# Performance work log

Hardware: AMD Instinct MI355X
Metric: run time of the kernel (lower is better)

Reference implementation:

```python
import jax, jax.numpy as jnp
import numpy as np

M, K, N, GROUP = 32, 8192, 28672, 128


def setup_inputs() -> dict:
    key = jax.random.key(0)
    k1, k2, k3, k4 = jax.random.split(key, 4)
    x = jax.random.normal(k1, (M, K), dtype=jnp.float16)
    # int32 words, each packing 8 consecutive int4 values along K
    qweight = jax.random.randint(k2, (K // 8, N), 0, 2147483647, dtype=jnp.int32)
    scales = (jax.random.uniform(k3, (K // GROUP, N), dtype=jnp.float32) * 0.01 + 0.001).astype(jnp.float16)
    bias = (jax.random.normal(k4, (N,), dtype=jnp.float32) * 0.02).astype(jnp.float16)
    return {"x": x, "qweight": qweight, "scales": scales, "bias": bias}


def reference(x, qweight, scales, bias):
    # Unpack 8 int4 nibbles per int32 word along K: (K//8, N) -> (K, N)
    K8, n = qweight.shape
    shifts = (jnp.arange(8, dtype=jnp.int32) * 4)[None, :, None]
    wq = ((qweight[:, None, :] >> shifts) & 15).reshape(K8 * 8, n)  # [K, N] in [0,15]
    # Dequant: zero-point fixed at 8 (pack() asserts zeros==8), per-group scales
    w = wq.astype(jnp.float16) - jnp.float16(8.0)
    g, gs = scales.shape[0], (K8 * 8) // scales.shape[0]
    w = (w.reshape(g, gs, n) * scales[:, None, :]).reshape(K8 * 8, n)  # [K, N] fp16
    return jnp.dot(x, w) + bias  # [M, N]
```

## Files before the change

kernel.cpp:

```cpp
#include <hip/hip_runtime.h>
#include <stdint.h>

#define K_DIM 8192
#define N_DIM 28672
#define NG    16

typedef _Float16 half8 __attribute__((ext_vector_type(8)));
typedef _Float16 half2t __attribute__((ext_vector_type(2)));
typedef float f32x16 __attribute__((ext_vector_type(16)));

__global__ __launch_bounds__(256) void prep_x(const float* __restrict__ x,
                                              _Float16* __restrict__ xp) {
  int idx = blockIdx.x * 256 + threadIdx.x;
  int m  = idx & 31;
  int k8 = idx >> 5;
  const float* p = x + (size_t)m * K_DIM + (size_t)k8 * 8;
  float4 xa = *(const float4*)p;
  float4 xb = *(const float4*)(p + 4);
  half2t p0 = __builtin_bit_cast(half2t, __builtin_amdgcn_cvt_pkrtz(xa.x, xb.x));
  half2t p1 = __builtin_bit_cast(half2t, __builtin_amdgcn_cvt_pkrtz(xa.y, xb.y));
  half2t p2 = __builtin_bit_cast(half2t, __builtin_amdgcn_cvt_pkrtz(xa.z, xb.z));
  half2t p3 = __builtin_bit_cast(half2t, __builtin_amdgcn_cvt_pkrtz(xa.w, xb.w));
  half8 o;
  o[0] = p0[0]; o[1] = p0[1]; o[2] = p1[0]; o[3] = p1[1];
  o[4] = p2[0]; o[5] = p2[1]; o[6] = p3[0]; o[7] = p3[1];
  *(half8*)(xp + ((size_t)k8 * 32 + m) * 8) = o;
}

static __device__ __forceinline__ half8 dqs(uint32_t w, half2t sh) {
  const uint32_t M4 = 0x000F000Fu, E = 0x64006400u;
  half2t off; off[0] = (_Float16)(-1032.0f); off[1] = (_Float16)(-1032.0f);
  half2t v0 = (__builtin_bit_cast(half2t, ( w        & M4) | E) + off) * sh;
  half2t v1 = (__builtin_bit_cast(half2t, ((w >> 4)  & M4) | E) + off) * sh;
  half2t v2 = (__builtin_bit_cast(half2t, ((w >> 8)  & M4) | E) + off) * sh;
  half2t v3 = (__builtin_bit_cast(half2t, ((w >> 12) & M4) | E) + off) * sh;
  half8 r;
  r[0] = v0[0]; r[1] = v0[1]; r[2] = v1[0]; r[3] = v1[1];
  r[4] = v2[0]; r[5] = v2[1]; r[6] = v3[0]; r[7] = v3[1];
  return r;
}

static __device__ __forceinline__ void waitcnt_vm8() { __builtin_amdgcn_s_waitcnt(0x0F78); }
static __device__ __forceinline__ void waitcnt_vm0() { __builtin_amdgcn_s_waitcnt(0x0F70); }

__global__ __launch_bounds__(256, 4) void qgemm(
    const uint32_t* __restrict__ q, const float* __restrict__ scales,
    const float* __restrict__ bias, const _Float16* __restrict__ xp,
    float* __restrict__ out) {
  __shared__ float red[4][16][64];
  const int tid  = threadIdx.x;
  const int w    = tid >> 6;
  const int lane = tid & 63;
  const int h    = lane >> 5;
  const int nl   = lane & 31;
  const int ct   = blockIdx.x;
  const int c0   = ct << 5;
  const int wr0  = w << 8;

  const uint32_t qb  = (uint32_t)((((uint64_t)(wr0 + h)) * N_DIM + c0 + nl) * 4);
  const uint32_t ab  = (uint32_t)(((wr0 + h) * 32 + nl) * 16);
  const uint32_t sb  = (uint32_t)((((uint64_t)(w * NG)) * N_DIM + c0 + nl) * 4);

  uint32_t qr[2][8];
  float4   aA[2][8];
  uint32_t sv[2];

  auto qload = [&](int g, int p) {
#pragma unroll
    for (int i = 0; i < 8; i++) {
      uint32_t vo = qb + (uint32_t)(g * 16 + 2 * i) * (uint32_t)(N_DIM * 4);
      asm volatile("global_load_dword %0, %1, %2"
                   : "=v"(qr[p][i]) : "v"(vo), "s"(q));
    }
  };
  auto aload = [&](int g, int p) {
#pragma unroll
    for (int i = 0; i < 8; i++) {
      uint32_t vo = ab + (uint32_t)(g * 8192 + i * 1024);
      asm volatile("global_load_dwordx4 %0, %1, %2"
                   : "=v"(aA[p][i]) : "v"(vo), "s"(xp));
    }
  };
  auto sload = [&](int g, int p) {
    uint32_t vo = sb + (uint32_t)g * (uint32_t)(N_DIM * 4);
    asm volatile("global_load_dword %0, %1, %2"
                 : "=v"(sv[p]) : "v"(vo), "s"(scales));
  };

  f32x16 acc;
#pragma unroll
  for (int j = 0; j < 16; j++) acc[j] = 0.0f;

  qload(0, 0); sload(0, 0); aload(0, 0); qload(1, 1);

  auto step = [&](int g, int p) {
    if (g == NG - 1) waitcnt_vm0(); else waitcnt_vm8();
    __builtin_amdgcn_sched_barrier(0);
    float sf = __builtin_bit_cast(float, sv[p]);
    half2t s2 = __builtin_bit_cast(half2t, __builtin_amdgcn_cvt_pkrtz(sf, sf));
#pragma unroll
    for (int i = 0; i < 8; i++) {
      acc = __builtin_amdgcn_mfma_f32_32x32x16_f16(
          __builtin_bit_cast(half8, aA[p][i]), dqs(qr[p][i], s2), acc, 0, 0, 0);
    }
    if (g + 1 < NG) { sload(g + 1, p ^ 1); aload(g + 1, p ^ 1); }
    if (g + 2 < NG) qload(g + 2, p);
  };

#pragma unroll 2
  for (int gg = 0; gg < NG; gg += 2) {
    step(gg, 0);
    step(gg + 1, 1);
  }

#pragma unroll
  for (int j = 0; j < 16; j++) red[w][j][lane] = acc[j];
  __syncthreads();

  float b = bias[c0 + nl];
#pragma unroll
  for (int jj = 0; jj < 4; jj++) {
    int j = w * 4 + jj;
    float v = red[0][j][lane] + red[1][j][lane] +
              red[2][j][lane] + red[3][j][lane];
    int row = (j & 3) + ((j >> 2) << 3) + (h << 2);
    out[(size_t)row * N_DIM + c0 + nl] = v + b;
  }
}

extern "C" void kernel_launch(void* const* d_in, const int* in_sizes, int n_in,
                              void* d_out, int out_size, void* d_ws, size_t ws_size,
                              hipStream_t stream) {
  const float*    xf      = (const float*)d_in[0];
  const uint32_t* qweight = (const uint32_t*)d_in[1];
  const float*    scales  = (const float*)d_in[2];
  const float*    bias    = (const float*)d_in[3];
  float*          out     = (float*)d_out;
  _Float16*       xp      = (_Float16*)d_ws;

  prep_x<<<dim3(128), dim3(256), 0, stream>>>(xf, xp);
  qgemm<<<dim3(N_DIM / 32), dim3(256), 0, stream>>>(qweight, scales, bias, xp, out);
}
```

Before: 208.8 us.

## Split K across eight waves per block, preload scales, stream activations per MFMA

Doubles the block to 512 threads so eight waves each cover 1024 K instead of 256 threads covering 2048, halving the sequential group loop per wave. All per-group scales are loaded up front into registers, and activation fragments are single-buffered and refilled one at a time right after each MFMA consumes them, freeing VGPRs. Launch bounds are raised to allow more resident waves. In exchange the cross-wave LDS reduction grows to eight partial sums, and the single-buffered activation loads have less slack to hide latency.

```diff
diff --git a/kernel.cpp b/kernel.cpp
--- a/kernel.cpp
+++ b/kernel.cpp
@@ -3,7 +3,7 @@
 
 #define K_DIM 8192
 #define N_DIM 28672
-#define NG    16
+#define NG    8
 
 typedef _Float16 half8 __attribute__((ext_vector_type(8)));
 typedef _Float16 half2t __attribute__((ext_vector_type(2)));
@@ -43,11 +43,11 @@
 static __device__ __forceinline__ void waitcnt_vm8() { __builtin_amdgcn_s_waitcnt(0x0F78); }
 static __device__ __forceinline__ void waitcnt_vm0() { __builtin_amdgcn_s_waitcnt(0x0F70); }
 
-__global__ __launch_bounds__(256, 4) void qgemm(
+__global__ __launch_bounds__(512, 6) void qgemm(
     const uint32_t* __restrict__ q, const float* __restrict__ scales,
     const float* __restrict__ bias, const _Float16* __restrict__ xp,
     float* __restrict__ out) {
-  __shared__ float red[4][16][64];
+  __shared__ float red[8][16][64];
   const int tid  = threadIdx.x;
   const int w    = tid >> 6;
   const int lane = tid & 63;
@@ -55,15 +55,22 @@
   const int nl   = lane & 31;
   const int ct   = blockIdx.x;
   const int c0   = ct << 5;
-  const int wr0  = w << 8;
+  const int wr0  = w << 7;
 
-  const uint32_t qb  = (uint32_t)((((uint64_t)(wr0 + h)) * N_DIM + c0 + nl) * 4);
-  const uint32_t ab  = (uint32_t)(((wr0 + h) * 32 + nl) * 16);
-  const uint32_t sb  = (uint32_t)((((uint64_t)(w * NG)) * N_DIM + c0 + nl) * 4);
+  half2t sh[8];
+#pragma unroll
+  for (int g = 0; g < NG; g++) {
+    float s = scales[(size_t)(w * NG + g) * N_DIM + c0 + nl];
+    sh[g] = __builtin_bit_cast(half2t, __builtin_amdgcn_cvt_pkrtz(s, s));
+  }
+  waitcnt_vm0();
+  __builtin_amdgcn_sched_barrier(0);
+
+  const uint32_t qb = (uint32_t)((((uint64_t)(wr0 + h)) * N_DIM + c0 + nl) * 4);
+  const uint32_t ab = (uint32_t)(((wr0 + h) * 32 + nl) * 16);
 
   uint32_t qr[2][8];
-  float4   aA[2][8];
-  uint32_t sv[2];
+  float4   aA[8];
 
   auto qload = [&](int g, int p) {
 #pragma unroll
@@ -73,44 +80,33 @@
                    : "=v"(qr[p][i]) : "v"(vo), "s"(q));
     }
   };
-  auto aload = [&](int g, int p) {
-#pragma unroll
-    for (int i = 0; i < 8; i++) {
-      uint32_t vo = ab + (uint32_t)(g * 8192 + i * 1024);
-      asm volatile("global_load_dwordx4 %0, %1, %2"
-                   : "=v"(aA[p][i]) : "v"(vo), "s"(xp));
-    }
-  };
-  auto sload = [&](int g, int p) {
-    uint32_t vo = sb + (uint32_t)g * (uint32_t)(N_DIM * 4);
-    asm volatile("global_load_dword %0, %1, %2"
-                 : "=v"(sv[p]) : "v"(vo), "s"(scales));
+  auto aload1 = [&](int g, int i) {
+    uint32_t vo = ab + (uint32_t)(g * 8192 + i * 1024);
+    asm volatile("global_load_dwordx4 %0, %1, %2"
+                 : "=v"(aA[i]) : "v"(vo), "s"(xp));
   };
 
   f32x16 acc;
 #pragma unroll
   for (int j = 0; j < 16; j++) acc[j] = 0.0f;
 
-  qload(0, 0); sload(0, 0); aload(0, 0); qload(1, 1);
+  qload(0, 0);
+#pragma unroll
+  for (int i = 0; i < 8; i++) aload1(0, i);
+  qload(1, 1);
 
-  auto step = [&](int g, int p) {
-    if (g == NG - 1) waitcnt_vm0(); else waitcnt_vm8();
+#pragma unroll
+  for (int g = 0; g < NG; g++) {
+    if (g < NG - 1) waitcnt_vm8(); else waitcnt_vm0();
     __builtin_amdgcn_sched_barrier(0);
-    float sf = __builtin_bit_cast(float, sv[p]);
-    half2t s2 = __builtin_bit_cast(half2t, __builtin_amdgcn_cvt_pkrtz(sf, sf));
+    half2t s = sh[g];
 #pragma unroll
     for (int i = 0; i < 8; i++) {
       acc = __builtin_amdgcn_mfma_f32_32x32x16_f16(
-          __builtin_bit_cast(half8, aA[p][i]), dqs(qr[p][i], s2), acc, 0, 0, 0);
+          __builtin_bit_cast(half8, aA[i]), dqs(qr[g & 1][i], s), acc, 0, 0, 0);
+      if (g + 1 < NG) aload1(g + 1, i);
     }
-    if (g + 1 < NG) { sload(g + 1, p ^ 1); aload(g + 1, p ^ 1); }
-    if (g + 2 < NG) qload(g + 2, p);
-  };
-
-#pragma unroll 2
-  for (int gg = 0; gg < NG; gg += 2) {
-    step(gg, 0);
-    step(gg + 1, 1);
+    if (g + 2 < NG) qload(g + 2, g & 1);
   }
 
 #pragma unroll
@@ -119,10 +115,11 @@
 
   float b = bias[c0 + nl];
 #pragma unroll
-  for (int jj = 0; jj < 4; jj++) {
-    int j = w * 4 + jj;
-    float v = red[0][j][lane] + red[1][j][lane] +
-              red[2][j][lane] + red[3][j][lane];
+  for (int jj = 0; jj < 2; jj++) {
+    int j = w * 2 + jj;
+    float v = red[0][j][lane] + red[1][j][lane] + red[2][j][lane] +
+              red[3][j][lane] + red[4][j][lane] + red[5][j][lane] +
+              red[6][j][lane] + red[7][j][lane];
     int row = (j & 3) + ((j >> 2) << 3) + (h << 2);
     out[(size_t)row * N_DIM + c0 + nl] = v + b;
   }
@@ -139,5 +136,5 @@
   _Float16*       xp      = (_Float16*)d_ws;
 
   prep_x<<<dim3(128), dim3(256), 0, stream>>>(xf, xp);
-  qgemm<<<dim3(N_DIM / 32), dim3(256), 0, stream>>>(qweight, scales, bias, xp, out);
+  qgemm<<<dim3(N_DIM / 32), dim3(512), 0, stream>>>(qweight, scales, bias, xp, out);
 }
```

Result: slower. 215.7 us (+3.3%).
